# Performance work log

Measured on AMD Instinct MI355X. Metric: run time of the kernel, lower is better.

Reference implementation:

```python
import jax, jax.numpy as jnp
import numpy as np

NUM_HEADS = 12
KSIZE = 3
PAD = 1


def setup_inputs() -> dict:
    key = jax.random.key(0)
    ks = jax.random.split(key, 5)
    B, H, W, C = 4, 96, 96, 192
    x = jax.random.normal(ks[0], (B, H * W, C), jnp.float32)
    Wq = jax.random.normal(ks[1], (W, W), jnp.float32) * 0.02
    bq = jnp.zeros((W,), jnp.float32)
    Wkv = jax.random.normal(ks[2], (2 * W, W), jnp.float32) * 0.02
    bkv = jnp.zeros((2 * W,), jnp.float32)
    Wp = jax.random.normal(ks[3], (C, C), jnp.float32) * 0.02
    bp = jnp.zeros((C,), jnp.float32)
    f_qr = jnp.float32(1.0)
    f_kr = jnp.float32(1.0)
    f_vr = jnp.float32(1.0)
    return {"x": x, "Wq": Wq, "bq": bq, "Wkv": Wkv, "bkv": bkv, "Wp": Wp,
            "bp": bp, "f_qr": f_qr, "f_kr": f_kr, "f_vr": f_vr, "H": H, "W": W}


def reference(x, Wq, bq, Wkv, bkv, Wp, bp, f_qr, f_kr, f_vr, H, W):
    B, N, C = x.shape
    nh = NUM_HEADS
    hc = C // nh
    scale = C ** (-0.5)
    # faithful to torch: raw reshape of (B, N, C) into (B, C, H, W)
    xn = x.reshape(B, C, H, W)
    # q_proj is Linear over the last (width) axis, size Hw == W
    q = jnp.einsum('bchw,vw->bchv', xn, Wq) + bq            # (B,C,H,W)
    q = q.reshape(B, H, W, nh, hc).transpose(0, 3, 1, 2, 4)  # (B,nh,H,W,hc)
    q = (q * scale * f_qr).reshape(B, nh, H * W, hc)         # (B,nh,L,hc)
    # kv_proj: Linear(W -> 2W) over last axis
    kv = jnp.einsum('bchw,vw->bchv', xn, Wkv) + bkv          # (B,C,H,2W)
    kv = kv.reshape(B, H, W, 2, nh, hc).transpose(3, 0, 4, 5, 1, 2)  # (2,B,nh,hc,H,W)
    kv = jnp.pad(kv, ((0, 0),) * 4 + ((PAD, PAD), (PAD, PAD)))       # zero-pad spatial
    # unfold: 3x3 sliding windows, stride 1 -> one window per pixel
    patches = jnp.stack([kv[..., i:i + H, j:j + W]
                         for i in range(KSIZE) for j in range(KSIZE)], axis=4)
    # (2,B,nh,hc,9,H,W) -> (2,B,nh,L,9,hc); kernel index = kh*3+kw matches nn.Unfold
    patches = patches.reshape(2, B, nh, hc, KSIZE * KSIZE, H * W).transpose(0, 1, 2, 5, 4, 3)
    k = patches[0] * f_kr                                    # (B,nh,L,9,hc)
    v = patches[1] * f_vr
    attn = jax.nn.softmax(jnp.einsum('bnlc,bnlkc->bnlk', q, k), axis=-1)  # (B,nh,L,9)
    out = jnp.einsum('bnlk,bnlkc->bnlc', attn, v)            # (B,nh,L,hc)
    out = out.transpose(0, 2, 1, 3).reshape(B, H, W, C)      # (B,H,W,C)
    out = jnp.einsum('bhwc,oc->bhwo', out, Wp) + bp          # proj Linear(dim,dim)
    return out.reshape(B, H * W, C)
```

## Files before the change

### kernel.cpp

```cpp
#include <hip/hip_runtime.h>

#define HW2   96
#define NH    12
#define LPIX  (HW2*HW2)
#define BATCH 4

typedef __attribute__((ext_vector_type(8))) short bf16x8;
typedef __attribute__((ext_vector_type(4))) float f32x4;

static __device__ __forceinline__ float bf2f(unsigned short u) {
  union { unsigned int i; float f; } v; v.i = ((unsigned int)u) << 16; return v.f;
}
static __device__ __forceinline__ unsigned short f2bf(float f) {
  union { float f; unsigned int i; } v; v.f = f;
  unsigned int r = v.i + 0x7FFF + ((v.i >> 16) & 1);
  return (unsigned short)(r >> 16);
}

__global__ __launch_bounds__(256) void cvt_w_kernel(
    const float* __restrict__ Wq, const float* __restrict__ Wkv,
    const float* __restrict__ Wp,
    unsigned short* __restrict__ wqb, unsigned short* __restrict__ wkvb,
    unsigned short* __restrict__ wpb) {
  int i = blockIdx.x * 256 + threadIdx.x;
  if (i < 9216)       wqb[i]          = f2bf(Wq[i]);
  else if (i < 27648) wkvb[i - 9216]  = f2bf(Wkv[i - 9216]);
  else if (i < 64512) wpb[i - 27648]  = f2bf(Wp[i - 27648]);
}

__global__ __launch_bounds__(256) void qkv_gemm(
    const float* __restrict__ X,
    const unsigned short* __restrict__ wq, const unsigned short* __restrict__ wkv,
    const float* __restrict__ bq, const float* __restrict__ bkv,
    const float* __restrict__ fqr, const float* __restrict__ fkr,
    const float* __restrict__ fvr,
    unsigned short* __restrict__ Qb, unsigned short* __restrict__ KVb)
{
  const int tid  = threadIdx.x;
  const int r0   = blockIdx.x * 128;
  const int lane = tid & 63, w = tid >> 6;
  const int col  = lane & 15;
  const int koff = (lane >> 4) * 8;
  const int arow0 = r0 + 16 * w + (lane & 15);
  const int rb0   = r0 + 16 * w + 4 * (lane >> 4);

  bf16x8 af[2][3];
  #pragma unroll
  for (int t = 0; t < 2; t++) {
    const float* xr = X + (size_t)(arow0 + 64 * t) * 96;
    float xv[24];
    *(float4*)&xv[0]  = *(const float4*)(xr + koff);
    *(float4*)&xv[4]  = *(const float4*)(xr + koff + 4);
    *(float4*)&xv[8]  = *(const float4*)(xr + koff + 32);
    *(float4*)&xv[12] = *(const float4*)(xr + koff + 36);
    *(float4*)&xv[16] = *(const float4*)(xr + koff + 64);
    *(float4*)&xv[20] = *(const float4*)(xr + koff + 68);
    unsigned short au[24];
    #pragma unroll
    for (int j = 0; j < 24; j++) au[j] = f2bf(xv[j]);
    af[t][0] = *(const bf16x8*)&au[0];
    af[t][1] = *(const bf16x8*)&au[8];
    af[t][2] = *(const bf16x8*)&au[16];
  }

  const float fqr0 = fqr[0] * 0.07216878364870322f;
  const float fkr0 = fkr[0], fvr0 = fvr[0];

  #pragma unroll
  for (int g = 0; g < 6; g++) {
    bf16x8 bw0[3], bw1[3], bw2[3];
    #pragma unroll
    for (int j = 0; j < 3; j++) {
      int nt = g * 3 + j;
      const unsigned short* wrow = (nt < 6)
          ? wq  + (size_t)(nt * 16 + col) * 96 + koff
          : wkv + (size_t)((nt - 6) * 16 + col) * 96 + koff;
      bw0[j] = *(const bf16x8*)(wrow);
      bw1[j] = *(const bf16x8*)(wrow + 32);
      bw2[j] = *(const bf16x8*)(wrow + 64);
    }
    asm volatile("" ::: "memory");

    #pragma unroll
    for (int j = 0; j < 3; j++) {
      int nt = g * 3 + j;
      f32x4 acc[2];
      #pragma unroll
      for (int t = 0; t < 2; t++) {
        f32x4 a = {0.f, 0.f, 0.f, 0.f};
        a = __builtin_amdgcn_mfma_f32_16x16x32_bf16(af[t][0], bw0[j], a, 0, 0, 0);
        a = __builtin_amdgcn_mfma_f32_16x16x32_bf16(af[t][1], bw1[j], a, 0, 0, 0);
        a = __builtin_amdgcn_mfma_f32_16x16x32_bf16(af[t][2], bw2[j], a, 0, 0, 0);
        acc[t] = a;
      }

      if (nt < 6) {
        int u = nt * 16 + col;
        float bias = bq[u];
        #pragma unroll
        for (int t = 0; t < 2; t++)
          #pragma unroll
          for (int i = 0; i < 4; i++)
            Qb[(size_t)(rb0 + 64 * t + i) * 96 + u] = f2bf((acc[t][i] + bias) * fqr0);
      } else {
        int u = (nt - 6) * 16 + col;
        float bias = bkv[u];
        #pragma unroll
        for (int t = 0; t < 2; t++)
          #pragma unroll
          for (int i = 0; i < 4; i++) {
            float s = (i & 1) ? fvr0 : fkr0;
            KVb[(size_t)(rb0 + 64 * t + i) * 192 + u] = f2bf((acc[t][i] + bias) * s);
          }
      }
    }
  }
}

__global__ __launch_bounds__(192, 1) void attnproj_kernel(
    const unsigned short* __restrict__ Qb, const unsigned short* __restrict__ KVb,
    const unsigned short* __restrict__ wp, const float* __restrict__ bp,
    float* __restrict__ Out)
{
  __shared__ unsigned short s_out[64 * 204];
  const int tid = threadIdx.x;
  const int bid = (blockIdx.x & 7) * 72 + (blockIdx.x >> 3);
  const int b   = bid / 144;
  const int rem = bid % 144;
  const int hp  = rem / 3, wt = rem % 3;
  const int h   = 2 * hp;
  const int w0  = 32 * wt;

  {
    const int n  = tid % NH;
    const int qd = tid / NH;
    const int w  = w0 + 2 * qd;

    const unsigned short* kvb = KVb + (size_t)b * (LPIX * 384) + n * 16;

    int nbo[16];
    #pragma unroll
    for (int hx = 0; hx < 16; hx++) {
      int hh = h + (hx >> 2) - 1;
      int ww = w + (hx & 3) - 1;
      int hc = min(max(hh, 0), HW2 - 1);
      int wc = min(max(ww, 0), HW2 - 1);
      nbo[hx] = (hc * HW2 + wc) * 384;
    }
    const bool rok[4] = { h > 0, true, true, h < HW2 - 2 };

    uint4 kH[16][2];
    #pragma unroll
    for (int hx = 0; hx < 16; hx++) {
      const unsigned short* kp = kvb + nbo[hx];
      kH[hx][0] = *(const uint4*)(kp);
      kH[hx][1] = *(const uint4*)(kp + 8);
    }
    uint4 qA[4], qB[4];
    #pragma unroll
    for (int t = 0; t < 4; t++) {
      int l = (h + (t >> 1)) * HW2 + w + (t & 1);
      const unsigned short* qp = Qb + ((size_t)b * LPIX + l) * 192 + n * 16;
      qA[t] = *(const uint4*)(qp);
      qB[t] = *(const uint4*)(qp + 8);
    }
    asm volatile("" ::: "memory");

    float sc[4][9];
    bool  okk[4][9];
    #pragma unroll
    for (int t = 0; t < 4; t++) {
      const int tr = t >> 1, tc = t & 1;
      float q[16];
      const unsigned short* qs = (const unsigned short*)&qA[t];
      #pragma unroll
      for (int j = 0; j < 8; j++) q[j] = bf2f(qs[j]);
      qs = (const unsigned short*)&qB[t];
      #pragma unroll
      for (int j = 0; j < 8; j++) q[8 + j] = bf2f(qs[j]);
      #pragma unroll
      for (int kk = 0; kk < 9; kk++) {
        int dr = kk / 3, dc = kk % 3;
        int hx = (dr + tr) * 4 + dc + tc;
        int wcol = w + tc + dc - 1;
        okk[t][kk] = rok[dr + tr] && ((unsigned)wcol < (unsigned)HW2);
        float s = 0.f;
        const unsigned short* kd = (const unsigned short*)&kH[hx][0];
        #pragma unroll
        for (int j = 0; j < 8; j++) s = fmaf(q[j], bf2f(kd[j]), s);
        kd = (const unsigned short*)&kH[hx][1];
        #pragma unroll
        for (int j = 0; j < 8; j++) s = fmaf(q[8 + j], bf2f(kd[j]), s);
        sc[t][kk] = okk[t][kk] ? s : 0.f;
      }
    }

    uint4 vH[16][2];
    #pragma unroll
    for (int hx = 0; hx < 16; hx++) {
      const unsigned short* vp = kvb + nbo[hx] + 192;
      vH[hx][0] = *(const uint4*)(vp);
      vH[hx][1] = *(const uint4*)(vp + 8);
    }
    asm volatile("" ::: "memory");

    #pragma unroll
    for (int t = 0; t < 4; t++) {
      const int tr = t >> 1, tc = t & 1;
      float m = sc[t][0];
      #pragma unroll
      for (int kk = 1; kk < 9; kk++) m = fmaxf(m, sc[t][kk]);
      float ssum = 0.f;
      #pragma unroll
      for (int kk = 0; kk < 9; kk++) {
        float e = __expf(sc[t][kk] - m);
        sc[t][kk] = e;
        ssum += e;
      }
      float acc[16];
      #pragma unroll
      for (int j = 0; j < 16; j++) acc[j] = 0.f;
      #pragma unroll
      for (int kk = 0; kk < 9; kk++) {
        int hx = (kk / 3 + tr) * 4 + kk % 3 + tc;
        float wgt = okk[t][kk] ? sc[t][kk] : 0.f;
        const unsigned short* vd = (const unsigned short*)&vH[hx][0];
        #pragma unroll
        for (int j = 0; j < 8; j++) acc[j] = fmaf(wgt, bf2f(vd[j]), acc[j]);
        vd = (const unsigned short*)&vH[hx][1];
        #pragma unroll
        for (int j = 0; j < 8; j++) acc[8 + j] = fmaf(wgt, bf2f(vd[j]), acc[8 + j]);
      }
      float rinv = 1.f / ssum;
      unsigned short od[16];
      #pragma unroll
      for (int j = 0; j < 16; j++) od[j] = f2bf(acc[j] * rinv);
      int sr = tr * 32 + 2 * qd + tc;
      unsigned short* op = s_out + sr * 204 + n * 16;
      *(uint4*)(op)     = *(uint4*)&od[0];
      *(uint4*)(op + 8) = *(uint4*)&od[8];
    }
  }
  __syncthreads();

  const int lane = tid & 63, wv = tid >> 6;
  const int col  = lane & 15;
  const int koff = (lane >> 4) * 8;

  bf16x8 af[4][6];
  #pragma unroll
  for (int rg = 0; rg < 4; rg++) {
    int arow = 16 * rg + (lane & 15);
    #pragma unroll
    for (int kt = 0; kt < 6; kt++)
      af[rg][kt] = *(const bf16x8*)&s_out[arow * 204 + koff + kt * 32];
  }

  #pragma unroll
  for (int t4 = 0; t4 < 4; t4++) {
    int nt = wv * 4 + t4;
    const unsigned short* wrow = wp + (size_t)(nt * 16 + col) * 192 + koff;
    bf16x8 bw[6];
    #pragma unroll
    for (int kt = 0; kt < 6; kt++) bw[kt] = *(const bf16x8*)(wrow + kt * 32);
    asm volatile("" ::: "memory");

    int u = nt * 16 + col;
    float bias = bp[u];
    #pragma unroll
    for (int rg = 0; rg < 4; rg++) {
      f32x4 acc = {0.f, 0.f, 0.f, 0.f};
      #pragma unroll
      for (int kt = 0; kt < 6; kt++)
        acc = __builtin_amdgcn_mfma_f32_16x16x32_bf16(af[rg][kt], bw[kt], acc, 0, 0, 0);
      int hh_out = h + (rg >> 1);
      int wbase  = w0 + 16 * (rg & 1) + 4 * (lane >> 4);
      #pragma unroll
      for (int i = 0; i < 4; i++) {
        int row_g = b * LPIX + hh_out * HW2 + wbase + i;
        Out[(size_t)row_g * 192 + u] = acc[i] + bias;
      }
    }
  }
}

extern "C" void kernel_launch(void* const* d_in, const int* in_sizes, int n_in,
                              void* d_out, int out_size, void* d_ws, size_t ws_size,
                              hipStream_t stream) {
  const float* x   = (const float*)d_in[0];
  const float* Wq  = (const float*)d_in[1];
  const float* bq  = (const float*)d_in[2];
  const float* Wkv = (const float*)d_in[3];
  const float* bkv = (const float*)d_in[4];
  const float* Wp  = (const float*)d_in[5];
  const float* bp  = (const float*)d_in[6];
  const float* fqr = (const float*)d_in[7];
  const float* fkr = (const float*)d_in[8];
  const float* fvr = (const float*)d_in[9];

  char* ws = (char*)d_ws;
  unsigned short* Qb   = (unsigned short*)ws;
  unsigned short* KVb  = (unsigned short*)(ws + 14155776);
  unsigned short* wqb  = (unsigned short*)(ws + 42467328);
  unsigned short* wkvb = (unsigned short*)(ws + 42485760);
  unsigned short* wpb  = (unsigned short*)(ws + 42522624);

  cvt_w_kernel<<<dim3(252), dim3(256), 0, stream>>>(Wq, Wkv, Wp, wqb, wkvb, wpb);

  qkv_gemm<<<dim3(576), dim3(256), 0, stream>>>(
      x, wqb, wkvb, bq, bkv, fqr, fkr, fvr, Qb, KVb);

  attnproj_kernel<<<dim3(576), dim3(192), 0, stream>>>(
      Qb, KVb, wpb, bp, (float*)d_out);
}
```

Measured before the change: 63.82 us.

## Fuse Q projection into attention kernel via LDS, drop global Q buffer

Moves the Q projection out of the QKV GEMM and into the attention+projection kernel. Each block computes its own 128 Q rows with MFMA into shared memory and reads them from there. The global Q buffer and its write and read round trip (about 14 MB of bf16) go away. In exchange, the attention kernel reads x rows again, adds extra MFMA work and barriers before attention, and reuses the LDS buffer for the output tile.

```diff
diff --git a/kernel.cpp b/kernel.cpp
--- a/kernel.cpp
+++ b/kernel.cpp
@@ -28,13 +28,11 @@
   else if (i < 64512) wpb[i - 27648]  = f2bf(Wp[i - 27648]);
 }
 
-__global__ __launch_bounds__(256) void qkv_gemm(
+__global__ __launch_bounds__(256) void kv_gemm(
     const float* __restrict__ X,
-    const unsigned short* __restrict__ wq, const unsigned short* __restrict__ wkv,
-    const float* __restrict__ bq, const float* __restrict__ bkv,
-    const float* __restrict__ fqr, const float* __restrict__ fkr,
-    const float* __restrict__ fvr,
-    unsigned short* __restrict__ Qb, unsigned short* __restrict__ KVb)
+    const unsigned short* __restrict__ wkv, const float* __restrict__ bkv,
+    const float* __restrict__ fkr, const float* __restrict__ fvr,
+    unsigned short* __restrict__ KVb)
 {
   const int tid  = threadIdx.x;
   const int r0   = blockIdx.x * 128;
@@ -63,18 +61,15 @@
     af[t][2] = *(const bf16x8*)&au[16];
   }
 
-  const float fqr0 = fqr[0] * 0.07216878364870322f;
   const float fkr0 = fkr[0], fvr0 = fvr[0];
 
   #pragma unroll
-  for (int g = 0; g < 6; g++) {
+  for (int g = 0; g < 4; g++) {
     bf16x8 bw0[3], bw1[3], bw2[3];
     #pragma unroll
     for (int j = 0; j < 3; j++) {
       int nt = g * 3 + j;
-      const unsigned short* wrow = (nt < 6)
-          ? wq  + (size_t)(nt * 16 + col) * 96 + koff
-          : wkv + (size_t)((nt - 6) * 16 + col) * 96 + koff;
+      const unsigned short* wrow = wkv + (size_t)(nt * 16 + col) * 96 + koff;
       bw0[j] = *(const bf16x8*)(wrow);
       bw1[j] = *(const bf16x8*)(wrow + 32);
       bw2[j] = *(const bf16x8*)(wrow + 64);
@@ -93,36 +88,30 @@
         a = __builtin_amdgcn_mfma_f32_16x16x32_bf16(af[t][2], bw2[j], a, 0, 0, 0);
         acc[t] = a;
       }
-
-      if (nt < 6) {
-        int u = nt * 16 + col;
-        float bias = bq[u];
-        #pragma unroll
-        for (int t = 0; t < 2; t++)
-          #pragma unroll
-          for (int i = 0; i < 4; i++)
-            Qb[(size_t)(rb0 + 64 * t + i) * 96 + u] = f2bf((acc[t][i] + bias) * fqr0);
-      } else {
-        int u = (nt - 6) * 16 + col;
-        float bias = bkv[u];
-        #pragma unroll
-        for (int t = 0; t < 2; t++)
-          #pragma unroll
-          for (int i = 0; i < 4; i++) {
-            float s = (i & 1) ? fvr0 : fkr0;
-            KVb[(size_t)(rb0 + 64 * t + i) * 192 + u] = f2bf((acc[t][i] + bias) * s);
-          }
-      }
+      int u = nt * 16 + col;
+      float bias = bkv[u];
+      #pragma unroll
+      for (int t = 0; t < 2; t++)
+        #pragma unroll
+        for (int i = 0; i < 4; i++) {
+          float s = (i & 1) ? fvr0 : fkr0;
+          KVb[(size_t)(rb0 + 64 * t + i) * 192 + u] = f2bf((acc[t][i] + bias) * s);
+        }
     }
   }
 }
 
 __global__ __launch_bounds__(192, 1) void attnproj_kernel(
-    const unsigned short* __restrict__ Qb, const unsigned short* __restrict__ KVb,
+    const float* __restrict__ X,
+    const unsigned short* __restrict__ wqb, const float* __restrict__ bq,
+    const float* __restrict__ fqr_p,
+    const unsigned short* __restrict__ KVb,
     const unsigned short* __restrict__ wp, const float* __restrict__ bp,
     float* __restrict__ Out)
 {
-  __shared__ unsigned short s_out[64 * 204];
+  __shared__ unsigned short q_lds[128 * 104];
+  unsigned short* s_out = q_lds;
+
   const int tid = threadIdx.x;
   const int bid = (blockIdx.x & 7) * 72 + (blockIdx.x >> 3);
   const int b   = bid / 144;
@@ -131,6 +120,70 @@
   const int h   = 2 * hp;
   const int w0  = 32 * wt;
 
+  const int lane = tid & 63;
+  const int col  = lane & 15;
+  const int koff = (lane >> 4) * 8;
+
+  {
+    const int wv = tid >> 6;
+    const size_t rr0 = (size_t)b * 18432 + (size_t)(h * 96 + w0) * 2;
+    const float fqr0 = fqr_p[0] * 0.07216878364870322f;
+
+    bf16x8 wf[2][3];
+    #pragma unroll
+    for (int c2 = 0; c2 < 2; c2++) {
+      int nt = wv * 2 + c2;
+      const unsigned short* wrow = wqb + (size_t)(nt * 16 + col) * 96 + koff;
+      wf[c2][0] = *(const bf16x8*)(wrow);
+      wf[c2][1] = *(const bf16x8*)(wrow + 32);
+      wf[c2][2] = *(const bf16x8*)(wrow + 64);
+    }
+
+    #pragma unroll
+    for (int rp = 0; rp < 4; rp++) {
+      float xv[2][24];
+      #pragma unroll
+      for (int r2 = 0; r2 < 2; r2++) {
+        int rt = rp * 2 + r2;
+        int lr = rt * 16 + (lane & 15);
+        const float* xr = X + (rr0 + (size_t)(lr >> 6) * 192 + (lr & 63)) * 96 + koff;
+        *(float4*)&xv[r2][0]  = *(const float4*)(xr);
+        *(float4*)&xv[r2][4]  = *(const float4*)(xr + 4);
+        *(float4*)&xv[r2][8]  = *(const float4*)(xr + 32);
+        *(float4*)&xv[r2][12] = *(const float4*)(xr + 36);
+        *(float4*)&xv[r2][16] = *(const float4*)(xr + 64);
+        *(float4*)&xv[r2][20] = *(const float4*)(xr + 68);
+      }
+      asm volatile("" ::: "memory");
+
+      #pragma unroll
+      for (int r2 = 0; r2 < 2; r2++) {
+        int rt = rp * 2 + r2;
+        unsigned short au[24];
+        #pragma unroll
+        for (int j = 0; j < 24; j++) au[j] = f2bf(xv[r2][j]);
+        bf16x8 a0 = *(const bf16x8*)&au[0];
+        bf16x8 a1 = *(const bf16x8*)&au[8];
+        bf16x8 a2 = *(const bf16x8*)&au[16];
+        int rloc = rt * 16 + 4 * (lane >> 4);
+        #pragma unroll
+        for (int c2 = 0; c2 < 2; c2++) {
+          int nt = wv * 2 + c2;
+          f32x4 acc = {0.f, 0.f, 0.f, 0.f};
+          acc = __builtin_amdgcn_mfma_f32_16x16x32_bf16(a0, wf[c2][0], acc, 0, 0, 0);
+          acc = __builtin_amdgcn_mfma_f32_16x16x32_bf16(a1, wf[c2][1], acc, 0, 0, 0);
+          acc = __builtin_amdgcn_mfma_f32_16x16x32_bf16(a2, wf[c2][2], acc, 0, 0, 0);
+          int u = nt * 16 + col;
+          float bias = bq[u];
+          #pragma unroll
+          for (int i = 0; i < 4; i++)
+            q_lds[(rloc + i) * 104 + u] = f2bf((acc[i] + bias) * fqr0);
+        }
+      }
+    }
+  }
+  __syncthreads();
+
   {
     const int n  = tid % NH;
     const int qd = tid / NH;
@@ -159,12 +212,14 @@
     uint4 qA[4], qB[4];
     #pragma unroll
     for (int t = 0; t < 4; t++) {
-      int l = (h + (t >> 1)) * HW2 + w + (t & 1);
-      const unsigned short* qp = Qb + ((size_t)b * LPIX + l) * 192 + n * 16;
-      qA[t] = *(const uint4*)(qp);
-      qB[t] = *(const uint4*)(qp + 8);
+      int tr = t >> 1, tc = t & 1;
+      int lr = tr * 64 + 2 * (2 * qd + tc) + (n >= 6 ? 1 : 0);
+      int u0 = (n % 6) * 16;
+      qA[t] = *(const uint4*)&q_lds[lr * 104 + u0];
+      qB[t] = *(const uint4*)&q_lds[lr * 104 + u0 + 8];
     }
     asm volatile("" ::: "memory");
+    __syncthreads();
 
     float sc[4][9];
     bool  okk[4][9];
@@ -243,42 +298,41 @@
   }
   __syncthreads();
 
-  const int lane = tid & 63, wv = tid >> 6;
-  const int col  = lane & 15;
-  const int koff = (lane >> 4) * 8;
-
-  bf16x8 af[4][6];
-  #pragma unroll
-  for (int rg = 0; rg < 4; rg++) {
-    int arow = 16 * rg + (lane & 15);
-    #pragma unroll
-    for (int kt = 0; kt < 6; kt++)
-      af[rg][kt] = *(const bf16x8*)&s_out[arow * 204 + koff + kt * 32];
-  }
-
-  #pragma unroll
-  for (int t4 = 0; t4 < 4; t4++) {
-    int nt = wv * 4 + t4;
-    const unsigned short* wrow = wp + (size_t)(nt * 16 + col) * 192 + koff;
-    bf16x8 bw[6];
-    #pragma unroll
-    for (int kt = 0; kt < 6; kt++) bw[kt] = *(const bf16x8*)(wrow + kt * 32);
-    asm volatile("" ::: "memory");
-
-    int u = nt * 16 + col;
-    float bias = bp[u];
+  {
+    const int wv = tid >> 6;
+    bf16x8 af[4][6];
     #pragma unroll
     for (int rg = 0; rg < 4; rg++) {
-      f32x4 acc = {0.f, 0.f, 0.f, 0.f};
+      int arow = 16 * rg + (lane & 15);
       #pragma unroll
       for (int kt = 0; kt < 6; kt++)
-        acc = __builtin_amdgcn_mfma_f32_16x16x32_bf16(af[rg][kt], bw[kt], acc, 0, 0, 0);
-      int hh_out = h + (rg >> 1);
-      int wbase  = w0 + 16 * (rg & 1) + 4 * (lane >> 4);
-      #pragma unroll
-      for (int i = 0; i < 4; i++) {
-        int row_g = b * LPIX + hh_out * HW2 + wbase + i;
-        Out[(size_t)row_g * 192 + u] = acc[i] + bias;
+        af[rg][kt] = *(const bf16x8*)&s_out[arow * 204 + koff + kt * 32];
+    }
+
+    #pragma unroll
+    for (int t4 = 0; t4 < 4; t4++) {
+      int nt = wv * 4 + t4;
+      const unsigned short* wrow = wp + (size_t)(nt * 16 + col) * 192 + koff;
+      bf16x8 bw[6];
+      #pragma unroll
+      for (int kt = 0; kt < 6; kt++) bw[kt] = *(const bf16x8*)(wrow + kt * 32);
+      asm volatile("" ::: "memory");
+
+      int u = nt * 16 + col;
+      float bias = bp[u];
+      #pragma unroll
+      for (int rg = 0; rg < 4; rg++) {
+        f32x4 acc = {0.f, 0.f, 0.f, 0.f};
+        #pragma unroll
+        for (int kt = 0; kt < 6; kt++)
+          acc = __builtin_amdgcn_mfma_f32_16x16x32_bf16(af[rg][kt], bw[kt], acc, 0, 0, 0);
+        int hh_out = h + (rg >> 1);
+        int wbase  = w0 + 16 * (rg & 1) + 4 * (lane >> 4);
+        #pragma unroll
+        for (int i = 0; i < 4; i++) {
+          int row_g = b * LPIX + hh_out * HW2 + wbase + i;
+          Out[(size_t)row_g * 192 + u] = acc[i] + bias;
+        }
       }
     }
   }
@@ -299,17 +353,16 @@
   const float* fvr = (const float*)d_in[9];
 
   char* ws = (char*)d_ws;
-  unsigned short* Qb   = (unsigned short*)ws;
-  unsigned short* KVb  = (unsigned short*)(ws + 14155776);
-  unsigned short* wqb  = (unsigned short*)(ws + 42467328);
-  unsigned short* wkvb = (unsigned short*)(ws + 42485760);
-  unsigned short* wpb  = (unsigned short*)(ws + 42522624);
+  unsigned short* KVb  = (unsigned short*)ws;
+  unsigned short* wqb  = (unsigned short*)(ws + 28311552);
+  unsigned short* wkvb = (unsigned short*)(ws + 28329984);
+  unsigned short* wpb  = (unsigned short*)(ws + 28366848);
 
   cvt_w_kernel<<<dim3(252), dim3(256), 0, stream>>>(Wq, Wkv, Wp, wqb, wkvb, wpb);
 
-  qkv_gemm<<<dim3(576), dim3(256), 0, stream>>>(
-      x, wqb, wkvb, bq, bkv, fqr, fkr, fvr, Qb, KVb);
+  kv_gemm<<<dim3(576), dim3(256), 0, stream>>>(
+      x, wkvb, bkv, fkr, fvr, KVb);
 
   attnproj_kernel<<<dim3(576), dim3(192), 0, stream>>>(
-      Qb, KVb, wpb, bp, (float*)d_out);
-}
+      x, wqb, bq, fqr, KVb, wpb, bp, (float*)d_out);
+}
```

Result: slower. 81.15 us (+27.2%).
